# Kernel optimization log

Measured on AMD Instinct MI355X. Metric: run time of the kernel, lower is better.

Reference implementation:

```python
import jax, jax.numpy as jnp
import numpy as np

HEADS = 8
FEATURE = 512
COMPUTE = 256
SEQ = 512
BATCH = 64


def setup_inputs() -> dict:
    key = jax.random.key(0)
    ks = jax.random.split(key, 10)
    d1 = jax.random.normal(ks[0], (BATCH, FEATURE), dtype=jnp.float32)
    d2 = jax.random.normal(ks[1], (SEQ, BATCH, FEATURE), dtype=jnp.float32)
    # linear1: Linear(FEATURE -> COMPUTE) + ReLU
    w1 = jax.random.normal(ks[2], (FEATURE, COMPUTE), dtype=jnp.float32) * (1.0 / np.sqrt(FEATURE))
    b1 = jnp.zeros((COMPUTE,), dtype=jnp.float32)
    # per-head score params, stacked: ws[i] is [2C, C], ps[i] is [C, 1]
    W = jax.random.normal(ks[3], (HEADS, 2 * COMPUTE, COMPUTE), dtype=jnp.float32)
    P = jax.random.normal(ks[4], (HEADS, COMPUTE), dtype=jnp.float32)
    # value projection weight_v: [FEATURE, COMPUTE]
    wv = jax.random.normal(ks[5], (FEATURE, COMPUTE), dtype=jnp.float32)
    # cc: Linear(COMPUTE*HEADS -> 128) + ReLU
    wcc = jax.random.normal(ks[6], (COMPUTE * HEADS, 128), dtype=jnp.float32) * (1.0 / np.sqrt(COMPUTE * HEADS))
    bcc = jnp.zeros((128,), dtype=jnp.float32)
    return {"d1": d1, "d2": d2, "w1": w1, "b1": b1, "W": W, "P": P,
            "wv": wv, "wcc": wcc, "bcc": bcc, "d2_size": SEQ}


def reference(d1, d2, w1, b1, W, P, wv, wcc, bcc, d2_size):
    S, B, F = d2.shape
    # linear1 on flattened d2 rows -> [S*B, C]
    d3 = jax.nn.relu(d2.reshape(-1, F) @ w1 + b1)
    # linear1 on d1, tiled S times along batch axis -> [S*B, C]
    d4 = jax.nn.relu(d1 @ w1 + b1)            # [B, C]
    d4 = jnp.tile(d4, (S, 1))                  # [S*B, C]
    d5 = jnp.concatenate([d3, d4], axis=1).reshape(S, B, -1)  # [S, B, 2C]
    # value path: tanh(d2 @ weight_v) -> [B, S, C]
    tv = jnp.tanh(jnp.einsum('sbf,fc->sbc', d2, wv)).transpose(1, 0, 2)
    # all heads batched: us = tanh(d5 @ W_h) -> [H, S, B, C]
    us = jnp.tanh(jnp.einsum('sbd,hdc->hsbc', d5, W))
    atts = jnp.einsum('hsbc,hc->hbs', us, P)   # [H, B, S]
    scores = jax.nn.softmax(atts, axis=-1)     # softmax over sequence
    vs = jnp.einsum('hbs,bsc->hbc', scores, tv)  # weighted sum over S -> [H, B, C]
    # torch.cat(vs, dim=1): head-major concat -> [B, H*C]
    vs = vs.transpose(1, 0, 2).reshape(B, -1)
    return jax.nn.relu(vs @ wcc + bcc)         # [B, 128]
```

## Files before the change

### kernel.cpp

```cpp
#include <hip/hip_runtime.h>
#include <cstddef>
#include <cstdint>

#define HH 8
#define FF 512
#define CC 256
#define SS 512
#define BB 64
#define SB (SS*BB)

typedef __attribute__((ext_vector_type(4))) float f32x4;
typedef __attribute__((ext_vector_type(8))) short bf16x8;

typedef __attribute__((address_space(1))) unsigned int gu32_t;
typedef __attribute__((address_space(3))) unsigned int lu32_t;

__device__ __forceinline__ void gld16(const void* gp, void* lp) {
    __builtin_amdgcn_global_load_lds((gu32_t*)gp, (lu32_t*)lp, 16, 0, 0);
}

__device__ __forceinline__ float fast_tanh(float x) {
    float e = __expf(2.0f * x);
    return 1.0f - 2.0f / (e + 1.0f);
}
__device__ __forceinline__ float relu_f(float x) { return fmaxf(x, 0.0f); }

__device__ __forceinline__ unsigned short f2bf(float x) {
    unsigned u = __float_as_uint(x);
    unsigned r = u + 0x7FFFu + ((u >> 16) & 1u);
    return (unsigned short)(r >> 16);
}
__device__ __forceinline__ float bf2f(unsigned short h) {
    return __uint_as_float(((unsigned)h) << 16);
}


__global__ __launch_bounds__(256) void p_prep(
    const float* __restrict__ w1, const float* __restrict__ wv,
    const float* __restrict__ W, const float* __restrict__ d1,
    const float* __restrict__ b1,
    unsigned short* __restrict__ w1ts, unsigned short* __restrict__ wvts,
    unsigned short* __restrict__ Wts, float* __restrict__ d4)
{
    __shared__ float T[64][65];
    __shared__ float As[16][68];
    __shared__ float Bs[16][68];
    const int tid = threadIdx.x;
    const int bid = blockIdx.x;
    if (bid < 192) {
        const float* src;
        unsigned short* dst;
        int kt64, nt;
        if (bid < 64) {
            int m = bid >> 5;
            int t = bid & 31;
            kt64 = t >> 2; nt = t & 3;
            src = m ? wv : w1;
            dst = m ? wvts : w1ts;
        } else {
            int t = bid - 64;
            int h = t >> 4; int tt = t & 15;
            kt64 = tt >> 2; nt = tt & 3;
            src = W + (size_t)h * 2 * CC * CC;
            dst = Wts + (size_t)h * 8 * CC * 64;
        }
        const int k0 = kt64 * 64, n0 = nt * 64;
        #pragma unroll
        for (int jj = 0; jj < 4; ++jj) {
            int i = (tid >> 4) + jj * 16;
            int j = (tid & 15) * 4;
            float4 v = *(const float4*)(src + (size_t)(k0 + i) * CC + n0 + j);
            T[i][j] = v.x; T[i][j+1] = v.y; T[i][j+2] = v.z; T[i][j+3] = v.w;
        }
        __syncthreads();
        {
            const int n_local = tid & 63;
            const int kg = (tid >> 6) * 16;
            const int n_abs = n0 + n_local;
            const int sxn = n_abs & 7;
            #pragma unroll
            for (int j = 0; j < 2; ++j) {
                const int kbase = kg + j * 8;
                const int k_abs = k0 + kbase;
                const int kt = k_abs >> 5;
                const int g = (k_abs >> 3) & 3;
                bf16x8 hv8, lv8;
                #pragma unroll
                for (int q = 0; q < 8; ++q) {
                    float x = T[kbase + q][n_local];
                    unsigned short hx = f2bf(x);
                    hv8[q] = (short)hx;
                    lv8[q] = (short)f2bf(x - bf2f(hx));
                }
                size_t rowo = ((size_t)kt * CC + n_abs) * 64;
                *(bf16x8*)(dst + rowo + (size_t)((2*g + 0) ^ sxn) * 8) = hv8;
                *(bf16x8*)(dst + rowo + (size_t)((2*g + 1) ^ sxn) * 8) = lv8;
            }
        }
    } else {
        const int n0 = (bid - 192) * 64;
        const int tx = tid & 15, ty = tid >> 4;
        const int lm = tid >> 2, lk4 = (tid & 3) * 4;
        const int bk = tid >> 4, bn4 = (tid & 15) * 4;
        float acc[4][4] = {};
        for (int k0 = 0; k0 < FF; k0 += 16) {
            float4 a = *(const float4*)(d1 + (size_t)lm * FF + k0 + lk4);
            As[lk4+0][lm] = a.x; As[lk4+1][lm] = a.y;
            As[lk4+2][lm] = a.z; As[lk4+3][lm] = a.w;
            *(float4*)&Bs[bk][bn4] = *(const float4*)(w1 + (size_t)(k0+bk)*CC + n0 + bn4);
            __syncthreads();
            #pragma unroll
            for (int kk = 0; kk < 16; ++kk) {
                float4 a4 = *(const float4*)&As[kk][ty*4];
                float4 b4 = *(const float4*)&Bs[kk][tx*4];
                float av[4] = {a4.x, a4.y, a4.z, a4.w};
                float bv[4] = {b4.x, b4.y, b4.z, b4.w};
                #pragma unroll
                for (int i = 0; i < 4; ++i)
                    #pragma unroll
                    for (int j = 0; j < 4; ++j)
                        acc[i][j] = fmaf(av[i], bv[j], acc[i][j]);
            }
            __syncthreads();
        }
        #pragma unroll
        for (int i = 0; i < 4; ++i) {
            int row = ty*4 + i;
            #pragma unroll
            for (int j = 0; j < 4; ++j)
                d4[(size_t)row*CC + n0 + tx*4 + j] = relu_f(acc[i][j] + b1[n0 + tx*4 + j]);
        }
    }
}

__global__ __launch_bounds__(256, 2) void k1_main(
    const float* __restrict__ d2,
    const unsigned short* __restrict__ w1ts, const unsigned short* __restrict__ wvts,
    const float* __restrict__ b1,
    const float* __restrict__ d4, const float* __restrict__ W,
    unsigned short* __restrict__ d3s, unsigned short* __restrict__ tv,
    float* __restrict__ e4)
{
    __shared__ __align__(16) unsigned short Abuf[128 * 64];
    __shared__ __align__(16) unsigned short Bbuf[256 * 64];

    const int tid = threadIdx.x;
    const int bid = blockIdx.x;

    if (bid >= 512) {
        float (*As)[68] = (float(*)[68])&Abuf[0];
        float (*Bs)[68] = (float(*)[68])&Bbuf[0];
        const int idx = bid - 512;
        const int n0 = (idx & 3) * 64;
        const int h  = idx >> 2;
        const float* Wh = W + ((size_t)h * 2 * CC + CC) * CC;
        const int tx = tid & 15, ty = tid >> 4;
        const int lm = tid >> 2, lk4 = (tid & 3) * 4;
        const int bk = tid >> 4, bn4 = (tid & 15) * 4;
        float acc[4][4] = {};
        for (int k0 = 0; k0 < CC; k0 += 16) {
            float4 a = *(const float4*)(d4 + (size_t)lm * CC + k0 + lk4);
            As[lk4+0][lm] = a.x; As[lk4+1][lm] = a.y;
            As[lk4+2][lm] = a.z; As[lk4+3][lm] = a.w;
            *(float4*)&Bs[bk][bn4] = *(const float4*)(Wh + (size_t)(k0+bk)*CC + n0 + bn4);
            __syncthreads();
            #pragma unroll
            for (int kk = 0; kk < 16; ++kk) {
                float4 a4 = *(const float4*)&As[kk][ty*4];
                float4 b4 = *(const float4*)&Bs[kk][tx*4];
                float av[4] = {a4.x, a4.y, a4.z, a4.w};
                float bv[4] = {b4.x, b4.y, b4.z, b4.w};
                #pragma unroll
                for (int i = 0; i < 4; ++i)
                    #pragma unroll
                    for (int j = 0; j < 4; ++j)
                        acc[i][j] = fmaf(av[i], bv[j], acc[i][j]);
            }
            __syncthreads();
        }
        #pragma unroll
        for (int i = 0; i < 4; ++i) {
            int b = ty*4 + i;
            #pragma unroll
            for (int j = 0; j < 4; ++j)
                e4[((size_t)h*BB + b)*CC + n0 + tx*4 + j] = acc[i][j];
        }
        return;
    }

    const int path = bid >> 8;
    const int r0 = (bid & 255) * 128;
    const int lane = tid & 63, w = tid >> 6;
    const int rowgrp = w & 1, colgrp = w >> 1;
    const int cb = lane & 15, quad = lane >> 4;
    const unsigned short* BT = path ? wvts : w1ts;

    f32x4 acc[4][8];
    f32x4 zero = {0.0f, 0.0f, 0.0f, 0.0f};
    #pragma unroll
    for (int rt = 0; rt < 4; ++rt)
        #pragma unroll
        for (int ct = 0; ct < 8; ++ct) acc[rt][ct] = zero;

    const int ar = tid >> 1, ak = (tid & 1) * 16;
    const int arx = ar & 7;
    const int g0 = ak >> 3;
    const int phi = (2 * quad) ^ (cb & 7);

    for (int k0 = 0; k0 < FF; k0 += 32) {
        const int kt = k0 >> 5;
        {
            const unsigned short* Bsrc = BT + (size_t)kt * (CC * 64);
            #pragma unroll
            for (int i = 0; i < 8; ++i) {
                int chunk = i * 4 + w;
                gld16(Bsrc + (size_t)chunk * 512 + lane * 8, &Bbuf[chunk * 512]);
            }
        }
        {
            const float* s = d2 + (size_t)(r0 + ar) * FF + k0 + ak;
            float v[16];
            *(float4*)&v[0]  = *(const float4*)(s);
            *(float4*)&v[4]  = *(const float4*)(s + 4);
            *(float4*)&v[8]  = *(const float4*)(s + 8);
            *(float4*)&v[12] = *(const float4*)(s + 12);
            bf16x8 vh0, vh1, vl0, vl1;
            #pragma unroll
            for (int j = 0; j < 8; ++j) {
                unsigned short h = f2bf(v[j]);
                vh0[j] = (short)h; vl0[j] = (short)f2bf(v[j] - bf2f(h));
                unsigned short h2 = f2bf(v[j+8]);
                vh1[j] = (short)h2; vl1[j] = (short)f2bf(v[j+8] - bf2f(h2));
            }
            unsigned short* Ar = &Abuf[ar * 64];
            *(bf16x8*)&Ar[((2*g0 + 0) ^ arx) * 8] = vh0;
            *(bf16x8*)&Ar[((2*g0 + 1) ^ arx) * 8] = vl0;
            *(bf16x8*)&Ar[((2*g0 + 2) ^ arx) * 8] = vh1;
            *(bf16x8*)&Ar[((2*g0 + 3) ^ arx) * 8] = vl1;
        }
        __syncthreads();
        bf16x8 ahf[4], alf[4];
        #pragma unroll
        for (int rt = 0; rt < 4; ++rt) {
            const unsigned short* Arow = &Abuf[(rowgrp*64 + rt*16 + cb) * 64];
            ahf[rt] = *(const bf16x8*)&Arow[phi * 8];
            alf[rt] = *(const bf16x8*)&Arow[(phi ^ 1) * 8];
        }
        #pragma unroll
        for (int ct = 0; ct < 8; ++ct) {
            const unsigned short* Brow = &Bbuf[(colgrp*128 + ct*16 + cb) * 64];
            bf16x8 bh = *(const bf16x8*)&Brow[phi * 8];
            bf16x8 bl = *(const bf16x8*)&Brow[(phi ^ 1) * 8];
            #pragma unroll
            for (int rt = 0; rt < 4; ++rt) {
                acc[rt][ct] = __builtin_amdgcn_mfma_f32_16x16x32_bf16(ahf[rt], bh, acc[rt][ct], 0, 0, 0);
                acc[rt][ct] = __builtin_amdgcn_mfma_f32_16x16x32_bf16(ahf[rt], bl, acc[rt][ct], 0, 0, 0);
                acc[rt][ct] = __builtin_amdgcn_mfma_f32_16x16x32_bf16(alf[rt], bh, acc[rt][ct], 0, 0, 0);
            }
        }
        __syncthreads();
    }
    if (path == 0) {
        float bias[8];
        #pragma unroll
        for (int ct = 0; ct < 8; ++ct) bias[ct] = b1[colgrp*128 + ct*16 + cb];
        #pragma unroll
        for (int rt = 0; rt < 4; ++rt) {
            #pragma unroll
            for (int r = 0; r < 4; ++r) {
                int gr = r0 + rowgrp*64 + rt*16 + quad*4 + r;
                int sxr = gr & 7;
                #pragma unroll
                for (int ct = 0; ct < 8; ++ct) {
                    int c = colgrp*128 + ct*16 + cb;
                    float val = relu_f(acc[rt][ct][r] + bias[ct]);
                    unsigned short hx = f2bf(val);
                    unsigned short lx = f2bf(val - bf2f(hx));
                    int kt = c >> 5;
                    int g = (c >> 3) & 3;
                    size_t rowo = ((size_t)kt * SB + gr) * 64;
                    d3s[rowo + (size_t)((2*g + 0) ^ sxr) * 8 + (c & 7)] = hx;
                    d3s[rowo + (size_t)((2*g + 1) ^ sxr) * 8 + (c & 7)] = lx;
                }
            }
        }
    } else {
        #pragma unroll
        for (int rt = 0; rt < 4; ++rt) {
            #pragma unroll
            for (int r = 0; r < 4; ++r) {
                int gr = r0 + rowgrp*64 + rt*16 + quad*4 + r;
                int s = gr >> 6, b = gr & 63;
                #pragma unroll
                for (int ct = 0; ct < 8; ++ct) {
                    int c = colgrp*128 + ct*16 + cb;
                    tv[((size_t)b * SS + s) * CC + c] = f2bf(fast_tanh(acc[rt][ct][r]));
                }
            }
        }
    }
}

__global__ __launch_bounds__(256, 2) void k3_atts(
    const unsigned short* __restrict__ d3s, const unsigned short* __restrict__ Wts,
    const float* __restrict__ e4, const float* __restrict__ P,
    float* __restrict__ atts)
{
    __shared__ __align__(16) unsigned short Abuf[128 * 64];
    __shared__ __align__(16) unsigned short Bbuf[256 * 64];
    __shared__ float red[2][128];

    const int tid = threadIdx.x;
    const int lane = tid & 63, w = tid >> 6;
    const int h = blockIdx.y;
    const int r0 = blockIdx.x * 128;
    const int rowgrp = w & 1, colgrp = w >> 1;
    const int cb = lane & 15, quad = lane >> 4;
    const int phi = (2 * quad) ^ (cb & 7);

    const unsigned short* Wh = Wts + (size_t)h * (8 * CC * 64);

    f32x4 acc[4][8];
    f32x4 zero = {0.0f, 0.0f, 0.0f, 0.0f};
    #pragma unroll
    for (int rt = 0; rt < 4; ++rt)
        #pragma unroll
        for (int ct = 0; ct < 8; ++ct) acc[rt][ct] = zero;

    for (int kt = 0; kt < 8; ++kt) {
        {
            const unsigned short* Asrc = d3s + ((size_t)kt * SB + r0) * 64;
            #pragma unroll
            for (int i = 0; i < 4; ++i) {
                int chunk = i * 4 + w;
                gld16(Asrc + (size_t)chunk * 512 + lane * 8, &Abuf[chunk * 512]);
            }
        }
        {
            const unsigned short* Bsrc = Wh + (size_t)kt * (CC * 64);
            #pragma unroll
            for (int i = 0; i < 8; ++i) {
                int chunk = i * 4 + w;
                gld16(Bsrc + (size_t)chunk * 512 + lane * 8, &Bbuf[chunk * 512]);
            }
        }
        __syncthreads();
        bf16x8 ahf[4], alf[4];
        #pragma unroll
        for (int rt = 0; rt < 4; ++rt) {
            const unsigned short* Arow = &Abuf[(rowgrp*64 + rt*16 + cb) * 64];
            ahf[rt] = *(const bf16x8*)&Arow[phi * 8];
            alf[rt] = *(const bf16x8*)&Arow[(phi ^ 1) * 8];
        }
        #pragma unroll
        for (int ct = 0; ct < 8; ++ct) {
            const unsigned short* Brow = &Bbuf[(colgrp*128 + ct*16 + cb) * 64];
            bf16x8 bh = *(const bf16x8*)&Brow[phi * 8];
            bf16x8 bl = *(const bf16x8*)&Brow[(phi ^ 1) * 8];
            #pragma unroll
            for (int rt = 0; rt < 4; ++rt) {
                acc[rt][ct] = __builtin_amdgcn_mfma_f32_16x16x32_bf16(ahf[rt], bh, acc[rt][ct], 0, 0, 0);
                acc[rt][ct] = __builtin_amdgcn_mfma_f32_16x16x32_bf16(ahf[rt], bl, acc[rt][ct], 0, 0, 0);
                acc[rt][ct] = __builtin_amdgcn_mfma_f32_16x16x32_bf16(alf[rt], bh, acc[rt][ct], 0, 0, 0);
            }
        }
        __syncthreads();
    }
    float Pv[8];
    #pragma unroll
    for (int ct = 0; ct < 8; ++ct) Pv[ct] = P[(size_t)h * CC + colgrp*128 + ct*16 + cb];
    #pragma unroll
    for (int rt = 0; rt < 4; ++rt) {
        #pragma unroll
        for (int r = 0; r < 4; ++r) {
            int b = rt*16 + quad*4 + r;
            const float* e4p = e4 + ((size_t)h * BB + b) * CC + colgrp*128 + cb;
            float part = 0.0f;
            #pragma unroll
            for (int ct = 0; ct < 8; ++ct) {
                float u = acc[rt][ct][r] + e4p[ct*16];
                part = fmaf(Pv[ct], fast_tanh(u), part);
            }
            part += __shfl_xor(part, 1); part += __shfl_xor(part, 2);
            part += __shfl_xor(part, 4); part += __shfl_xor(part, 8);
            if (cb == 0) red[colgrp][rowgrp*64 + b] = part;
        }
    }
    __syncthreads();
    if (tid < 128) {
        float v = red[0][tid] + red[1][tid];
        int gr = r0 + tid;
        int s = gr >> 6, b = gr & 63;
        atts[((size_t)h * BB + b) * SS + s] = v;
    }
}

__global__ __launch_bounds__(256) void k456_out(
    const float* __restrict__ atts, const unsigned short* __restrict__ tv,
    const float* __restrict__ wcc, const float* __restrict__ bcc,
    float* __restrict__ out)
{
    __shared__ float sc[HH][SS];
    __shared__ float red[4][2048];
    const int b = blockIdx.x;
    const int tid = threadIdx.x;
    const int lane = tid & 63, w = tid >> 6;

    for (int i = tid; i < HH*SS; i += 256) {
        int h = i >> 9, s = i & 511;
        sc[h][s] = atts[((size_t)h*BB + b)*SS + s];
    }
    __syncthreads();
    #pragma unroll
    for (int t = 0; t < 2; ++t) {
        int hh = w*2 + t;
        float x[8];
        #pragma unroll
        for (int j = 0; j < 8; ++j) x[j] = sc[hh][j*64 + lane];
        float m = x[0];
        #pragma unroll
        for (int j = 1; j < 8; ++j) m = fmaxf(m, x[j]);
        #pragma unroll
        for (int d = 1; d < 64; d <<= 1) m = fmaxf(m, __shfl_xor(m, d));
        float sum = 0.0f;
        #pragma unroll
        for (int j = 0; j < 8; ++j) { x[j] = __expf(x[j] - m); sum += x[j]; }
        #pragma unroll
        for (int d = 1; d < 64; d <<= 1) sum += __shfl_xor(sum, d);
        float inv = 1.0f / sum;
        #pragma unroll
        for (int j = 0; j < 8; ++j) sc[hh][j*64 + lane] = x[j] * inv;
    }
    __syncthreads();
    {
        const int cl = tid & 63, stripe = tid >> 6;
        const int c0 = cl * 4;
        const unsigned short* tvb = tv + ((size_t)b * SS + stripe * 128) * CC + c0;
        float acc[HH][4] = {};
        for (int si = 0; si < 128; ++si) {
            uint2 u = *(const uint2*)(tvb + (size_t)si * CC);
            float x0 = bf2f((unsigned short)(u.x));
            float x1 = bf2f((unsigned short)(u.x >> 16));
            float x2 = bf2f((unsigned short)(u.y));
            float x3 = bf2f((unsigned short)(u.y >> 16));
            int s = stripe * 128 + si;
            #pragma unroll
            for (int h = 0; h < HH; ++h) {
                float wgt = sc[h][s];
                acc[h][0] = fmaf(wgt, x0, acc[h][0]);
                acc[h][1] = fmaf(wgt, x1, acc[h][1]);
                acc[h][2] = fmaf(wgt, x2, acc[h][2]);
                acc[h][3] = fmaf(wgt, x3, acc[h][3]);
            }
        }
        #pragma unroll
        for (int h = 0; h < HH; ++h)
            #pragma unroll
            for (int j = 0; j < 4; ++j)
                red[stripe][h*256 + c0 + j] = acc[h][j];
    }
    __syncthreads();
    for (int i = tid; i < 2048; i += 256)
        red[0][i] = red[0][i] + red[1][i] + red[2][i] + red[3][i];
    __syncthreads();
    {
        const int n = tid & 127, half = tid >> 7;
        float o = 0.0f;
        const int kbase = half * 1024;
        for (int k = 0; k < 1024; ++k)
            o = fmaf(red[0][kbase + k], wcc[(size_t)(kbase + k) * 128 + n], o);
        float* r2 = &sc[0][0];
        r2[half * 128 + n] = o;
    }
    __syncthreads();
    if (tid < 128)
        out[(size_t)b * 128 + tid] = relu_f(sc[0][tid] + sc[0][128 + tid] + bcc[tid]);
}

extern "C" void kernel_launch(void* const* d_in, const int* in_sizes, int n_in,
                              void* d_out, int out_size, void* d_ws, size_t ws_size,
                              hipStream_t stream)
{
    (void)in_sizes; (void)n_in; (void)out_size; (void)ws_size;
    const float* d1  = (const float*)d_in[0];
    const float* d2  = (const float*)d_in[1];
    const float* w1  = (const float*)d_in[2];
    const float* b1  = (const float*)d_in[3];
    const float* W   = (const float*)d_in[4];
    const float* P   = (const float*)d_in[5];
    const float* wv  = (const float*)d_in[6];
    const float* wcc = (const float*)d_in[7];
    const float* bcc = (const float*)d_in[8];
    float* out = (float*)d_out;

    char* p = (char*)d_ws;
    unsigned short* d3s  = (unsigned short*)p; p += (size_t)8 * SB * 64 * 2;
    unsigned short* tv   = (unsigned short*)p; p += (size_t)SB * CC * 2;
    unsigned short* w1ts = (unsigned short*)p; p += (size_t)16 * CC * 64 * 2;
    unsigned short* wvts = (unsigned short*)p; p += (size_t)16 * CC * 64 * 2;
    unsigned short* Wts  = (unsigned short*)p; p += (size_t)HH * 8 * CC * 64 * 2;
    float* d4   = (float*)p;  p += (size_t)BB * CC * 4;
    float* e4   = (float*)p;  p += (size_t)HH * BB * CC * 4;
    float* atts = (float*)p;  p += (size_t)HH * BB * SS * 4;

    p_prep   <<<dim3(196),       256, 0, stream>>>(w1, wv, W, d1, b1,
                  w1ts, wvts, Wts, d4);
    k1_main  <<<dim3(544),       256, 0, stream>>>(d2, w1ts, wvts, b1, d4, W,
                  d3s, tv, e4);
    k3_atts  <<<dim3(256, HH),   256, 0, stream>>>(d3s, Wts, e4, P, atts);
    k456_out <<<dim3(BB),        256, 0, stream>>>(atts, tv, wcc, bcc, out);
}
```

Before: 367.1 us.

## Double-buffer k3_atts LDS tiles and enlarge block to 256 rows

The attention-score GEMM kernel now uses 512 threads per block and a 256-row tile, so each W tile staged in LDS is reused across twice as many rows. It double-buffers the A and B tiles in LDS and issues the next k-step's global-to-LDS loads before computing the current one. The MFMA section runs at raised wave priority. The aim is to hide global load latency and cut redundant weight traffic, at the cost of about 130KB of LDS, which allows only one block per CU.

```diff
diff --git a/kernel.cpp b/kernel.cpp
--- a/kernel.cpp
+++ b/kernel.cpp
@@ -301,20 +301,20 @@
     }
 }
 
-__global__ __launch_bounds__(256, 2) void k3_atts(
+__global__ __launch_bounds__(512, 2) void k3_atts(
     const unsigned short* __restrict__ d3s, const unsigned short* __restrict__ Wts,
     const float* __restrict__ e4, const float* __restrict__ P,
     float* __restrict__ atts)
 {
-    __shared__ __align__(16) unsigned short Abuf[128 * 64];
-    __shared__ __align__(16) unsigned short Bbuf[256 * 64];
-    __shared__ float red[2][128];
+    __shared__ __align__(16) unsigned short Abuf[2][256 * 64];
+    __shared__ __align__(16) unsigned short Bbuf[2][256 * 64];
+    __shared__ float red[2][256];
 
     const int tid = threadIdx.x;
     const int lane = tid & 63, w = tid >> 6;
     const int h = blockIdx.y;
-    const int r0 = blockIdx.x * 128;
-    const int rowgrp = w & 1, colgrp = w >> 1;
+    const int r0 = blockIdx.x * 256;
+    const int rowgrp = w & 3, colgrp = w >> 2;
     const int cb = lane & 15, quad = lane >> 4;
     const int phi = (2 * quad) ^ (cb & 7);
 
@@ -327,34 +327,33 @@
         #pragma unroll
         for (int ct = 0; ct < 8; ++ct) acc[rt][ct] = zero;
 
-    for (int kt = 0; kt < 8; ++kt) {
-        {
-            const unsigned short* Asrc = d3s + ((size_t)kt * SB + r0) * 64;
-            #pragma unroll
-            for (int i = 0; i < 4; ++i) {
-                int chunk = i * 4 + w;
-                gld16(Asrc + (size_t)chunk * 512 + lane * 8, &Abuf[chunk * 512]);
-            }
-        }
-        {
-            const unsigned short* Bsrc = Wh + (size_t)kt * (CC * 64);
-            #pragma unroll
-            for (int i = 0; i < 8; ++i) {
-                int chunk = i * 4 + w;
-                gld16(Bsrc + (size_t)chunk * 512 + lane * 8, &Bbuf[chunk * 512]);
-            }
-        }
-        __syncthreads();
+    auto STAGE = [&](int buf, int kt) {
+        const unsigned short* Asrc = d3s + ((size_t)kt * SB + r0) * 64;
+        const unsigned short* Bsrc = Wh + (size_t)kt * (CC * 64);
+        #pragma unroll
+        for (int i = 0; i < 4; ++i) {
+            int chunk = i * 8 + w;
+            gld16(Asrc + (size_t)chunk * 512 + lane * 8, &Abuf[buf][chunk * 512]);
+        }
+        #pragma unroll
+        for (int i = 0; i < 4; ++i) {
+            int chunk = i * 8 + w;
+            gld16(Bsrc + (size_t)chunk * 512 + lane * 8, &Bbuf[buf][chunk * 512]);
+        }
+    };
+
+    auto COMPUTE = [&](int buf) {
         bf16x8 ahf[4], alf[4];
         #pragma unroll
         for (int rt = 0; rt < 4; ++rt) {
-            const unsigned short* Arow = &Abuf[(rowgrp*64 + rt*16 + cb) * 64];
+            const unsigned short* Arow = &Abuf[buf][(rowgrp*64 + rt*16 + cb) * 64];
             ahf[rt] = *(const bf16x8*)&Arow[phi * 8];
             alf[rt] = *(const bf16x8*)&Arow[(phi ^ 1) * 8];
         }
+        __builtin_amdgcn_s_setprio(1);
         #pragma unroll
         for (int ct = 0; ct < 8; ++ct) {
-            const unsigned short* Brow = &Bbuf[(colgrp*128 + ct*16 + cb) * 64];
+            const unsigned short* Brow = &Bbuf[buf][(colgrp*128 + ct*16 + cb) * 64];
             bf16x8 bh = *(const bf16x8*)&Brow[phi * 8];
             bf16x8 bl = *(const bf16x8*)&Brow[(phi ^ 1) * 8];
             #pragma unroll
@@ -364,8 +363,25 @@
                 acc[rt][ct] = __builtin_amdgcn_mfma_f32_16x16x32_bf16(alf[rt], bh, acc[rt][ct], 0, 0, 0);
             }
         }
-        __syncthreads();
-    }
+        __builtin_amdgcn_s_setprio(0);
+    };
+
+    STAGE(0, 0);
+    asm volatile("s_waitcnt vmcnt(0)" ::: "memory");
+    __builtin_amdgcn_s_barrier();
+    __builtin_amdgcn_sched_barrier(0);
+
+    #pragma unroll
+    for (int kt = 0; kt < 8; ++kt) {
+        if (kt < 7) STAGE((kt + 1) & 1, kt + 1);
+        COMPUTE(kt & 1);
+        if (kt < 7) {
+            asm volatile("s_waitcnt vmcnt(0)" ::: "memory");
+            __builtin_amdgcn_s_barrier();
+            __builtin_amdgcn_sched_barrier(0);
+        }
+    }
+
     float Pv[8];
     #pragma unroll
     for (int ct = 0; ct < 8; ++ct) Pv[ct] = P[(size_t)h * CC + colgrp*128 + ct*16 + cb];
@@ -387,7 +403,7 @@
         }
     }
     __syncthreads();
-    if (tid < 128) {
+    if (tid < 256) {
         float v = red[0][tid] + red[1][tid];
         int gr = r0 + tid;
         int s = gr >> 6, b = gr & 63;
@@ -507,6 +523,6 @@
                   w1ts, wvts, Wts, d4);
     k1_main  <<<dim3(544),       256, 0, stream>>>(d2, w1ts, wvts, b1, d4, W,
                   d3s, tv, e4);
-    k3_atts  <<<dim3(256, HH),   256, 0, stream>>>(d3s, Wts, e4, P, atts);
+    k3_atts  <<<dim3(128, HH),   512, 0, stream>>>(d3s, Wts, e4, P, atts);
     k456_out <<<dim3(BB),        256, 0, stream>>>(atts, tv, wcc, bcc, out);
 }
```

Result: no change. 367.9 us (+0.2%).
